# Performance work log

Measured on AMD Instinct MI355X. Metric: run time of the kernel, lower is better.

## Reference

```python
import jax, jax.numpy as jnp
import numpy as np

UFEAT_DIM = 512
EFEAT_DIM = 256
BATCH = 64
PNUM_UNIT = 1024
PNUM_ENEMY = 1024


def setup_inputs() -> dict:
    key = jax.random.key(0)
    k1, k2, k3, k4, k5 = jax.random.split(key, 5)
    ufeat = jax.random.normal(k1, (BATCH, PNUM_UNIT, UFEAT_DIM), dtype=jnp.float32)
    efeat = jax.random.normal(k2, (BATCH, PNUM_ENEMY, EFEAT_DIM), dtype=jnp.float32)
    num_enemy = jax.random.randint(k3, (BATCH,), 0, PNUM_ENEMY, dtype=jnp.int64)
    # weight_norm(Linear, dim=None): W = g * v / ||v||_F, g scalar
    v = jax.random.normal(k4, (EFEAT_DIM, UFEAT_DIM), dtype=jnp.float32) * (1.0 / np.sqrt(UFEAT_DIM))
    g = jnp.asarray(jnp.linalg.norm(v), dtype=jnp.float32)  # init g = ||v||
    b = jax.random.normal(k5, (EFEAT_DIM,), dtype=jnp.float32) * 0.01
    return {"ufeat": ufeat, "efeat": efeat, "num_enemy": num_enemy, "v": v, "g": g, "b": b}


def reference(ufeat, efeat, num_enemy, v, g, b):
    # weight-normed linear (dim=None -> Frobenius norm) + ReLU projection
    W = g * v / jnp.linalg.norm(v)                       # [efeat_dim, ufeat_dim]
    proj = jax.nn.relu(ufeat @ W.T + b)                  # [B, U, efeat_dim]
    # batched dot-product scores (fused matmul instead of repeat+mul+sum)
    norm = jnp.float32(np.sqrt(EFEAT_DIM))
    logit = jnp.einsum('bue,bne->bun', proj, efeat) / norm  # [B, U, N]
    # real-enemy mask: mask[b, n] = 1 iff n < num_enemy[b]
    mask = (jnp.arange(PNUM_ENEMY)[None, :] < num_enemy[:, None]).astype(logit.dtype)
    logit = logit - (1.0 - mask)[:, None, :] * 1e9       # masking bias (uniform if all masked)
    prob = jax.nn.softmax(logit, axis=2)
    return prob
```

## Files before the change

kernel.cpp:

```cpp
#include <hip/hip_runtime.h>
#include <hip/hip_bf16.h>

#define UF 512
#define EF 256
#define NB 64
#define NU 1024
#define NEN 1024

typedef __attribute__((ext_vector_type(8))) short short8;
typedef __attribute__((ext_vector_type(4))) float floatx4;
typedef __attribute__((ext_vector_type(2))) _Float16 half2v;

typedef unsigned short ushort_t;

__device__ inline short2 cvt2(float a, float b) {
    __hip_bfloat162 h = __float22bfloat162_rn(make_float2(a, b));
    union { __hip_bfloat162 h; short2 s; } u;
    u.h = h;
    return u.s;
}

__device__ inline short8 cvt8v(floatx4 x, floatx4 y) {
    union { short8 v; short2 s[4]; } u;
    u.s[0] = cvt2(x[0], x[1]);
    u.s[1] = cvt2(x[2], x[3]);
    u.s[2] = cvt2(y[0], y[1]);
    u.s[3] = cvt2(y[2], y[3]);
    return u.v;
}

__device__ inline ushort_t f2bfbits(float f) {
    unsigned u = __float_as_uint(f);
    u += 0x7FFFu + ((u >> 16) & 1u);
    return (ushort_t)(u >> 16);
}

__global__ void knorm(const float* __restrict__ v, float* __restrict__ ws0) {
    int t = blockIdx.x * 256 + threadIdx.x;
    float2 x = ((const float2*)v)[t];
    float s = x.x * x.x + x.y * x.y;
    #pragma unroll
    for (int m = 1; m < 64; m <<= 1) s += __shfl_xor(s, m);
    __shared__ float ls[4];
    int w = threadIdx.x >> 6;
    if ((threadIdx.x & 63) == 0) ls[w] = s;
    __syncthreads();
    if (threadIdx.x == 0) atomicAdd(ws0, ls[0] + ls[1] + ls[2] + ls[3]);
}

__global__ void kconv(const float* __restrict__ v, const float* __restrict__ g,
                      const float* __restrict__ ef, const float* __restrict__ ws0,
                      const int* __restrict__ nen,
                      ushort_t* __restrict__ wsW, ushort_t* __restrict__ wsE) {
    int bid = blockIdx.x;
    if (bid < 128) {
        int t = bid * 256 + threadIdx.x;
        float s = g[0] * rsqrtf(ws0[0]);
        float4 x = ((const float4*)v)[t];
        short2 a = cvt2(x.x * s, x.y * s);
        short2 b = cvt2(x.z * s, x.w * s);
        ushort4 o;
        o.x = (ushort_t)a.x; o.y = (ushort_t)a.y; o.z = (ushort_t)b.x; o.w = (ushort_t)b.y;
        ((ushort4*)wsW)[t] = o;
    } else {
        long t = (long)(bid - 128) * 256 + threadIdx.x;
        int row = (int)(t >> 6);
        int n = row & (NEN - 1);
        int b = row >> 10;
        if (n < nen[b]) {
            floatx4 x = __builtin_nontemporal_load((const floatx4*)ef + t);
            short2 a = cvt2(x[0], x[1]);
            short2 c = cvt2(x[2], x[3]);
            ushort4 o;
            o.x = (ushort_t)a.x; o.y = (ushort_t)a.y; o.z = (ushort_t)c.x; o.w = (ushort_t)c.y;
            ((ushort4*)wsE)[t] = o;
        }
    }
}

__launch_bounds__(256, 2)
__global__ void kfused(const float* __restrict__ A, const ushort_t* __restrict__ W,
                       const float* __restrict__ bias, const ushort_t* __restrict__ E,
                       const int* __restrict__ nen, float* __restrict__ out) {
    const int tid = threadIdx.x;
    const int w = tid >> 6, L = tid & 63;
    const int rA = L & 15, q = L >> 4;
    const int bid = blockIdx.x;
    const int b = bid >> 5;
    const int ut = bid & 31;
    const int ne = nen[b];

    __shared__ ushort_t Pl[32][264];
    __shared__ float lsum[4][32];

    {
        const long m0 = (long)b * NU + (long)ut * 32;
        floatx4 acc[2][4];
        #pragma unroll
        for (int m = 0; m < 2; m++)
            #pragma unroll
            for (int n = 0; n < 4; n++) acc[m][n] = (floatx4){0.f, 0.f, 0.f, 0.f};

        const float* a0 = A + (m0 + rA) * UF + q * 8;
        const float* a1 = A + (m0 + 16 + rA) * UF + q * 8;
        const ushort_t* wp[4];
        #pragma unroll
        for (int n = 0; n < 4; n++) wp[n] = W + (long)(w * 64 + n * 16 + rA) * UF + q * 8;

        floatx4 x0 = *(const floatx4*)(a0);
        floatx4 y0 = *(const floatx4*)(a0 + 4);
        floatx4 x1 = *(const floatx4*)(a1);
        floatx4 y1 = *(const floatx4*)(a1 + 4);

        #pragma unroll 2
        for (int s = 0; s < 16; s++) {
            const int ko = s * 32;
            short8 wf[4];
            #pragma unroll
            for (int n = 0; n < 4; n++) wf[n] = *(const short8*)(wp[n] + ko);
            short8 af0 = cvt8v(x0, y0);
            short8 af1 = cvt8v(x1, y1);
            if (s < 15) {
                x0 = *(const floatx4*)(a0 + ko + 32);
                y0 = *(const floatx4*)(a0 + ko + 36);
                x1 = *(const floatx4*)(a1 + ko + 32);
                y1 = *(const floatx4*)(a1 + ko + 36);
            }
            #pragma unroll
            for (int n = 0; n < 4; n++) {
                acc[0][n] = __builtin_amdgcn_mfma_f32_16x16x32_bf16(af0, wf[n], acc[0][n], 0, 0, 0);
                acc[1][n] = __builtin_amdgcn_mfma_f32_16x16x32_bf16(af1, wf[n], acc[1][n], 0, 0, 0);
            }
        }

        #pragma unroll
        for (int n = 0; n < 4; n++) {
            const int col = w * 64 + n * 16 + rA;
            const float bv = bias[col];
            #pragma unroll
            for (int m = 0; m < 2; m++) {
                #pragma unroll
                for (int i = 0; i < 4; i++) {
                    float val = acc[m][n][i] + bv;
                    val = fmaxf(val, 0.f);
                    Pl[m * 16 + q * 4 + i][col] = f2bfbits(val);
                }
            }
        }
    }
    __syncthreads();

    short8 af[2][8];
    #pragma unroll
    for (int t = 0; t < 2; t++)
        #pragma unroll
        for (int s = 0; s < 8; s++)
            af[t][s] = *(const short8*)&Pl[t * 16 + rA][s * 32 + q * 8];

    half2v acc[2][16][2];
    #pragma unroll
    for (int t = 0; t < 2; t++)
        #pragma unroll
        for (int ns = 0; ns < 16; ns++) {
            acc[t][ns][0] = (half2v){(_Float16)0.f, (_Float16)0.f};
            acc[t][ns][1] = (half2v){(_Float16)0.f, (_Float16)0.f};
        }
    float psum[2][4];
    #pragma unroll
    for (int t = 0; t < 2; t++)
        #pragma unroll
        for (int i = 0; i < 4; i++) psum[t][i] = 0.f;

    const ushort_t* erow = E + (long)(b * NEN + w * 16 + rA) * EF + q * 8;

    short8 bf[2][8];
    if (w * 16 < ne) {
        #pragma unroll
        for (int s = 0; s < 8; s++) bf[0][s] = *(const short8*)(erow + s * 32);
    }

    #pragma unroll
    for (int ns = 0; ns < 16; ns++) {
        const int col0 = ns * 64 + w * 16;
        if (col0 < ne) {
            const int cur = ns & 1;
            if (ns < 15) {
                const ushort_t* epn = erow + (long)(ns + 1) * 64 * EF;
                #pragma unroll
                for (int s = 0; s < 8; s++) bf[cur ^ 1][s] = *(const short8*)(epn + s * 32);
            }
            floatx4 c0 = (floatx4){0.f, 0.f, 0.f, 0.f};
            floatx4 c1 = (floatx4){0.f, 0.f, 0.f, 0.f};
            #pragma unroll
            for (int s = 0; s < 8; s++) {
                c0 = __builtin_amdgcn_mfma_f32_16x16x32_bf16(af[0][s], bf[cur][s], c0, 0, 0, 0);
                c1 = __builtin_amdgcn_mfma_f32_16x16x32_bf16(af[1][s], bf[cur][s], c1, 0, 0, 0);
            }
            const int col = col0 + rA;
            const bool on = col < ne;
            #pragma unroll
            for (int i = 0; i < 4; i++) {
                float e0 = on ? __expf(c0[i] * 0.0625f) : 0.f;
                float e1 = on ? __expf(c1[i] * 0.0625f) : 0.f;
                psum[0][i] += e0; psum[1][i] += e1;
                c0[i] = e0; c1[i] = e1;
            }
            acc[0][ns][0] = (half2v){(_Float16)c0[0], (_Float16)c0[1]};
            acc[0][ns][1] = (half2v){(_Float16)c0[2], (_Float16)c0[3]};
            acc[1][ns][0] = (half2v){(_Float16)c1[0], (_Float16)c1[1]};
            acc[1][ns][1] = (half2v){(_Float16)c1[2], (_Float16)c1[3]};
        }
    }

    #pragma unroll
    for (int t = 0; t < 2; t++)
        #pragma unroll
        for (int i = 0; i < 4; i++) {
            float s = psum[t][i];
            s += __shfl_xor(s, 1);
            s += __shfl_xor(s, 2);
            s += __shfl_xor(s, 4);
            s += __shfl_xor(s, 8);
            psum[t][i] = s;
        }
    if (rA == 0) {
        #pragma unroll
        for (int t = 0; t < 2; t++)
            #pragma unroll
            for (int i = 0; i < 4; i++)
                lsum[w][t * 16 + q * 4 + i] = psum[t][i];
    }
    __syncthreads();

    float inv[2][4];
    #pragma unroll
    for (int t = 0; t < 2; t++)
        #pragma unroll
        for (int i = 0; i < 4; i++) {
            const int r = t * 16 + q * 4 + i;
            const float tot = lsum[0][r] + lsum[1][r] + lsum[2][r] + lsum[3][r];
            inv[t][i] = (ne > 0) ? (1.f / tot) : 0.f;
        }

    const float uni = 1.f / 1024.f;
    float* orow = out + ((long)(b * NU + ut * 32)) * (long)NEN + w * 16;
    #pragma unroll
    for (int ns = 0; ns < 16; ns++) {
        #pragma unroll
        for (int t = 0; t < 2; t++) {
            #pragma unroll
            for (int i = 0; i < 4; i++) {
                const int u = t * 16 + q * 4 + i;
                const float num = (float)acc[t][ns][i >> 1][i & 1];
                const float val = (ne == 0) ? uni : num * inv[t][i];
                __builtin_nontemporal_store(val, &orow[(long)u * NEN + ns * 64 + rA]);
            }
        }
    }
}

extern "C" void kernel_launch(void* const* d_in, const int* in_sizes, int n_in,
                              void* d_out, int out_size, void* d_ws, size_t ws_size,
                              hipStream_t stream) {
    (void)in_sizes; (void)n_in; (void)out_size; (void)ws_size;
    const float* ufeat = (const float*)d_in[0];
    const float* efeat = (const float*)d_in[1];
    const int*   nen   = (const int*)d_in[2];
    const float* v     = (const float*)d_in[3];
    const float* g     = (const float*)d_in[4];
    const float* bias  = (const float*)d_in[5];
    float* out = (float*)d_out;

    float*    ws0 = (float*)d_ws;
    ushort_t* wsW = (ushort_t*)((char*)d_ws + 1024);
    ushort_t* wsE = (ushort_t*)((char*)d_ws + (1u << 20));

    hipMemsetAsync(d_ws, 0, 256, stream);
    knorm<<<256, 256, 0, stream>>>(v, ws0);
    kconv<<<16512, 256, 0, stream>>>(v, g, efeat, ws0, nen, wsW, wsE);
    kfused<<<2048, 256, 0, stream>>>(ufeat, wsW, bias, wsE, nen, out);
}
```

Measured before the change: 563.7 us.

## Spill half of softmax numerators to LDS and raise occupancy to three blocks

Half of the fp16 exp numerators (the second 16-row tile) now go to a shared-memory buffer instead of registers, and launch bounds go from 2 to 3 blocks per CU. The aim is to cut VGPR pressure so more waves can hide the memory latency of the large output write. The W-fragment loads in the first GEMM are also double-buffered one k-step ahead. The cost is about 35KB more LDS per block plus extra LDS traffic, which may itself cap occupancy, and the prefetch adds registers.

```diff
diff --git a/kernel.cpp b/kernel.cpp
--- a/kernel.cpp
+++ b/kernel.cpp
@@ -10,6 +10,7 @@
 typedef __attribute__((ext_vector_type(8))) short short8;
 typedef __attribute__((ext_vector_type(4))) float floatx4;
 typedef __attribute__((ext_vector_type(2))) _Float16 half2v;
+typedef __attribute__((ext_vector_type(4))) _Float16 half4v;
 
 typedef unsigned short ushort_t;
 
@@ -78,7 +79,7 @@
     }
 }
 
-__launch_bounds__(256, 2)
+__launch_bounds__(256, 3)
 __global__ void kfused(const float* __restrict__ A, const ushort_t* __restrict__ W,
                        const float* __restrict__ bias, const ushort_t* __restrict__ E,
                        const int* __restrict__ nen, float* __restrict__ out) {
@@ -91,6 +92,7 @@
     const int ne = nen[b];
 
     __shared__ ushort_t Pl[32][264];
+    __shared__ ushort_t accL[256][68];
     __shared__ float lsum[4][32];
 
     {
@@ -111,13 +113,14 @@
         floatx4 y0 = *(const floatx4*)(a0 + 4);
         floatx4 x1 = *(const floatx4*)(a1);
         floatx4 y1 = *(const floatx4*)(a1 + 4);
+        short8 wf[2][4];
+        #pragma unroll
+        for (int n = 0; n < 4; n++) wf[0][n] = *(const short8*)(wp[n]);
 
         #pragma unroll 2
         for (int s = 0; s < 16; s++) {
+            const int cur = s & 1;
             const int ko = s * 32;
-            short8 wf[4];
-            #pragma unroll
-            for (int n = 0; n < 4; n++) wf[n] = *(const short8*)(wp[n] + ko);
             short8 af0 = cvt8v(x0, y0);
             short8 af1 = cvt8v(x1, y1);
             if (s < 15) {
@@ -125,11 +128,13 @@
                 y0 = *(const floatx4*)(a0 + ko + 36);
                 x1 = *(const floatx4*)(a1 + ko + 32);
                 y1 = *(const floatx4*)(a1 + ko + 36);
+                #pragma unroll
+                for (int n = 0; n < 4; n++) wf[cur ^ 1][n] = *(const short8*)(wp[n] + ko + 32);
             }
             #pragma unroll
             for (int n = 0; n < 4; n++) {
-                acc[0][n] = __builtin_amdgcn_mfma_f32_16x16x32_bf16(af0, wf[n], acc[0][n], 0, 0, 0);
-                acc[1][n] = __builtin_amdgcn_mfma_f32_16x16x32_bf16(af1, wf[n], acc[1][n], 0, 0, 0);
+                acc[0][n] = __builtin_amdgcn_mfma_f32_16x16x32_bf16(af0, wf[cur][n], acc[0][n], 0, 0, 0);
+                acc[1][n] = __builtin_amdgcn_mfma_f32_16x16x32_bf16(af1, wf[cur][n], acc[1][n], 0, 0, 0);
             }
         }
 
@@ -157,14 +162,12 @@
         for (int s = 0; s < 8; s++)
             af[t][s] = *(const short8*)&Pl[t * 16 + rA][s * 32 + q * 8];
 
-    half2v acc[2][16][2];
-    #pragma unroll
-    for (int t = 0; t < 2; t++)
-        #pragma unroll
-        for (int ns = 0; ns < 16; ns++) {
-            acc[t][ns][0] = (half2v){(_Float16)0.f, (_Float16)0.f};
-            acc[t][ns][1] = (half2v){(_Float16)0.f, (_Float16)0.f};
-        }
+    half2v acc0[16][2];
+    #pragma unroll
+    for (int ns = 0; ns < 16; ns++) {
+        acc0[ns][0] = (half2v){(_Float16)0.f, (_Float16)0.f};
+        acc0[ns][1] = (half2v){(_Float16)0.f, (_Float16)0.f};
+    }
     float psum[2][4];
     #pragma unroll
     for (int t = 0; t < 2; t++)
@@ -205,10 +208,10 @@
                 psum[0][i] += e0; psum[1][i] += e1;
                 c0[i] = e0; c1[i] = e1;
             }
-            acc[0][ns][0] = (half2v){(_Float16)c0[0], (_Float16)c0[1]};
-            acc[0][ns][1] = (half2v){(_Float16)c0[2], (_Float16)c0[3]};
-            acc[1][ns][0] = (half2v){(_Float16)c1[0], (_Float16)c1[1]};
-            acc[1][ns][1] = (half2v){(_Float16)c1[2], (_Float16)c1[3]};
+            acc0[ns][0] = (half2v){(_Float16)c0[0], (_Float16)c0[1]};
+            acc0[ns][1] = (half2v){(_Float16)c0[2], (_Float16)c0[3]};
+            half4v h1 = {(_Float16)c1[0], (_Float16)c1[1], (_Float16)c1[2], (_Float16)c1[3]};
+            *(half4v*)&accL[tid][ns * 4] = h1;
         }
     }
 
@@ -246,15 +249,19 @@
     float* orow = out + ((long)(b * NU + ut * 32)) * (long)NEN + w * 16;
     #pragma unroll
     for (int ns = 0; ns < 16; ns++) {
-        #pragma unroll
-        for (int t = 0; t < 2; t++) {
-            #pragma unroll
-            for (int i = 0; i < 4; i++) {
-                const int u = t * 16 + q * 4 + i;
-                const float num = (float)acc[t][ns][i >> 1][i & 1];
-                const float val = (ne == 0) ? uni : num * inv[t][i];
-                __builtin_nontemporal_store(val, &orow[(long)u * NEN + ns * 64 + rA]);
-            }
+        const bool act = (ns * 64 + w * 16) < ne;
+        half4v h1 = {(_Float16)0.f, (_Float16)0.f, (_Float16)0.f, (_Float16)0.f};
+        if (act) h1 = *(const half4v*)&accL[tid][ns * 4];
+        #pragma unroll
+        for (int i = 0; i < 4; i++) {
+            const int u0 = q * 4 + i;
+            const float n0 = (float)acc0[ns][i >> 1][i & 1];
+            const float v0 = (ne == 0) ? uni : n0 * inv[0][i];
+            __builtin_nontemporal_store(v0, &orow[(long)u0 * NEN + ns * 64 + rA]);
+            const int u1 = 16 + q * 4 + i;
+            const float n1 = (float)h1[i];
+            const float v1 = (ne == 0) ? uni : n1 * inv[1][i];
+            __builtin_nontemporal_store(v1, &orow[(long)u1 * NEN + ns * 64 + rA]);
         }
     }
 }
```

Measured after the change: 611.8 us. +8.5%, slower.
